# Optimization experiments

Hardware: AMD Instinct MI355X
Metric: run time of the kernel (lower is better)

Reference implementation:

```python
import jax, jax.numpy as jnp
import numpy as np

G, B, K, D = 16384, 4, 2, 64
NEG = -1e30


def _mlp3(x, w1, b1, w2, b2, w3, b3):
    # MLP: linear->relu x3 (BatchNorm defined but unused in original forward)
    h = jax.nn.relu(x @ w1 + b1)
    h = jax.nn.relu(h @ w2 + b2)
    return jax.nn.relu(h @ w3 + b3)


def setup_inputs() -> dict:
    key = jax.random.key(0)
    ks = jax.random.split(key, 32)

    def lin(k, fan_in, fan_out):
        k1, k2 = jax.random.split(k)
        s = 1.0 / np.sqrt(fan_in)
        w = jax.random.uniform(k1, (fan_in, fan_out), jnp.float32, -s, s)
        b = jax.random.uniform(k2, (fan_out,), jnp.float32, -s, s)
        return w, b

    inp = {}
    inp['ap_feat'] = jax.random.normal(ks[0], (G, B, 1), jnp.float32)
    inp['e_feat'] = jax.random.normal(ks[1], (G, B, K, 2), jnp.float32)
    inp['w_pre_ap'], inp['b_pre_ap'] = lin(ks[2], 1, D)
    inp['w_pre_edge'], inp['b_pre_edge'] = lin(ks[3], 2, D)
    # mlp_update_5 (AP-side neighbor messages), _6 (UE-side), _7 (edge update)
    inp['w5_1'], inp['b5_1'] = lin(ks[4], 2 * D, D)
    inp['w5_2'], inp['b5_2'] = lin(ks[5], D, D)
    inp['w5_3'], inp['b5_3'] = lin(ks[6], D, D)
    inp['w6_1'], inp['b6_1'] = lin(ks[7], 2 * D, D)
    inp['w6_2'], inp['b6_2'] = lin(ks[8], D, D)
    inp['w6_3'], inp['b6_3'] = lin(ks[9], D, D)
    inp['w7_1'], inp['b7_1'] = lin(ks[10], 2 * D, D)
    inp['w7_2'], inp['b7_2'] = lin(ks[11], D, D)
    inp['w7_3'], inp['b7_3'] = lin(ks[12], D, D)
    inp['w_post'], inp['b_post'] = lin(ks[13], D, 2)
    return inp


def _edge_conv(e, a, w5_1, b5_1, w5_2, b5_2, w5_3, b5_3,
               w6_1, b6_1, w6_2, b6_2, w6_3, b6_3,
               w7_1, b7_1, w7_2, b7_2, w7_3, b7_3):
    # e: [G,B,K,D] AP2UE edge hid; a: [G,B,D] AP hid.
    # M1[g,b,j] = mlp5(cat(a[g,b], e[g,b,j])) -- same-AP neighbor edges
    x1 = jnp.concatenate([jnp.broadcast_to(a[:, :, None, :], e.shape), e], axis=-1)  # [G,B,K,2D]
    M1 = _mlp3(x1, w5_1, b5_1, w5_2, b5_2, w5_3, b5_3)  # [G,B,K,D]
    # M2[g,b,bp,k] = mlp6(cat(a[g,b], e[g,bp,k])) -- same-UE neighbor edges
    # (original uses the SRC AP feature here too). Split first linear to
    # avoid materializing the [G,B,B,K,2D] concat.
    h = jax.nn.relu(
        (a @ w6_1[:D])[:, :, None, None, :]
        + (e @ w6_1[D:])[:, None, :, :, :]
        + b6_1)  # [G,B,B,K,D]
    h = jax.nn.relu(h @ w6_2 + b6_2)
    M2 = jax.nn.relu(h @ w6_3 + b6_3)  # [G,B,Bp,K,D]
    # masked max excluding the edge itself
    eyeK = jnp.eye(K, dtype=bool)  # [k, j]
    m1max = jnp.max(jnp.where(eyeK[None, None, :, :, None], NEG,
                              M1[:, :, None, :, :]), axis=3)  # [G,B,K,D]
    eyeB = jnp.eye(B, dtype=bool)  # [b, bp]
    m2max = jnp.max(jnp.where(eyeB[None, :, :, None, None], NEG, M2), axis=2)  # [G,B,K,D]
    agg = jnp.maximum(m1max, m2max)
    # new edge feature: mlp7(cat(agg, e_hid))
    return _mlp3(jnp.concatenate([agg, e], axis=-1),
                 w7_1, b7_1, w7_2, b7_2, w7_3, b7_3)


def reference(ap_feat, e_feat, w_pre_ap, b_pre_ap, w_pre_edge, b_pre_edge,
              w5_1, b5_1, w5_2, b5_2, w5_3, b5_3,
              w6_1, b6_1, w6_2, b6_2, w6_3, b6_3,
              w7_1, b7_1, w7_2, b7_2, w7_3, b7_3,
              w_post, b_post):
    # PreLayer (live branches only: AP nodes and AP2UE edges; APConv/UEConv
    # write node 'new' which is never read, so UE/UE2AP branches are dead).
    a = jax.nn.relu(ap_feat @ w_pre_ap + b_pre_ap)   # [G,B,D]
    e = jax.nn.relu(e_feat @ w_pre_edge + b_pre_edge)  # [G,B,K,D]
    # two UpdateLayers (shared weights: ModuleList([UpdateLayer()]*2) + global MLPs)
    for _ in range(2):
        e = _edge_conv(e, a, w5_1, b5_1, w5_2, b5_2, w5_3, b5_3,
                       w6_1, b6_1, w6_2, b6_2, w6_3, b6_3,
                       w7_1, b7_1, w7_2, b7_2, w7_3, b7_3)
    out = e @ w_post + b_post  # [G,B,K,2]
    r, im = out[..., 0], out[..., 1]
    # norm_func: per-graph [B,K] complex matrix, each row (over K) L2-normalized
    n = jnp.sqrt(jnp.sum(r * r + im * im, axis=-1, keepdims=True))
    return jnp.stack([r / n, im / n], axis=-1)  # [G,B,K,2]
```

## Files before the change

kernel.cpp:

```cpp
#include <hip/hip_runtime.h>


typedef unsigned short u16;
typedef unsigned int   u32;
typedef __attribute__((ext_vector_type(8))) short short8_t;
typedef __attribute__((ext_vector_type(2))) short short2v;
typedef __attribute__((ext_vector_type(4))) float floatx4;

#define OFF_W51 0
#define OFF_W61 8192
#define OFF_W71 16384
#define OFF_W52 24576
#define OFF_W53 28672
#define OFF_W62 32768
#define OFF_W63 36864
#define OFF_W72 40960
#define OFF_W73 45056
#define WS_U16  49152

#define CB51 0
#define CB52 64
#define CB53 128
#define CB61 192
#define CB62 256
#define CB63 320
#define CB71 384
#define CB72 448
#define CB73 512
#define CWPO 576
#define CBPO 704
#define CWPA 768
#define CBPA 832
#define CWPE 896
#define CBPE 1024
#define CSZ  1088

#define BUF_U16 1152
#define APB_U16 576
#define PW_U16  3456

struct Params {
  const float *ap, *ef;
  const float *wpa, *bpa, *wpe, *bpe;
  const float *w51, *b51, *w52, *b52, *w53, *b53;
  const float *w61, *b61, *w62, *b62, *w63, *b63;
  const float *w71, *b71, *w72, *b72, *w73, *b73;
  const float *wpost, *bpost;
  float *out;
  int gtot;
};

__device__ __forceinline__ u32 pk2(float a, float b) {
  const u32 ua = __float_as_uint(a) + 0x8000u;
  const u32 ub = __float_as_uint(b) + 0x8000u;
  return __builtin_amdgcn_perm(ub, ua, 0x07060302u);
}
__device__ __forceinline__ float blo(u32 v) { return __uint_as_float(v << 16); }
__device__ __forceinline__ float bhi(u32 v) { return __uint_as_float(v & 0xffff0000u); }
__device__ __forceinline__ u32 pkmax(u32 a, u32 b) {
  const short2v r = __builtin_elementwise_max(__builtin_bit_cast(short2v, a),
                                              __builtin_bit_cast(short2v, b));
  return __builtin_bit_cast(u32, r);
}
__device__ __forceinline__ u32 ror16(u32 x) { return (x >> 16) | (x << 16); }
__device__ __forceinline__ float sel4(int i, float x0, float x1, float x2, float x3) {
  const float lo = (i & 1) ? x1 : x0;
  const float hi = (i & 1) ? x3 : x2;
  return (i & 2) ? hi : lo;
}

__device__ __forceinline__ int skr(int row) { return row * 8 + (row >> 3) * 8; }

__device__ __forceinline__ floatx4 mfma16(short8_t a, short8_t b, floatx4 c) {
  return __builtin_amdgcn_mfma_f32_16x16x32_bf16(a, b, c, 0, 0, 0);
}
__device__ __forceinline__ short8_t ldAr(const u16* buf, int row) {
  return *(const short8_t*)(buf + skr(row));
}

template<int TSTRIDE>
__device__ __forceinline__ void layerK64R2(floatx4* aX, floatx4* aY,
                                           short8_t x0, short8_t x1,
                                           short8_t y0, short8_t y1,
                                           const u16* B, int l) {
#pragma unroll
  for (int t = 0; t < 4; ++t) {
    const short8_t b0 = *(const short8_t*)(B + (t * TSTRIDE + 0) * 512 + l * 8);
    const short8_t b1 = *(const short8_t*)(B + (t * TSTRIDE + 1) * 512 + l * 8);
    aX[t] = mfma16(x0, b0, aX[t]);
    aY[t] = mfma16(y0, b0, aY[t]);
    aX[t] = mfma16(x1, b1, aX[t]);
    aY[t] = mfma16(y1, b1, aY[t]);
  }
}

__device__ __forceinline__ void layerK128R2(floatx4* aX, floatx4* aY,
                                            const short8_t* fx, const short8_t* fy,
                                            const u16* B, int l) {
#pragma unroll
  for (int t = 0; t < 4; ++t)
#pragma unroll
    for (int h = 0; h < 4; ++h) {
      const short8_t b = *(const short8_t*)(B + (t * 4 + h) * 512 + l * 8);
      aX[t] = mfma16(fx[h], b, aX[t]);
      aY[t] = mfma16(fy[h], b, aY[t]);
    }
}

__device__ __forceinline__ void scatter_relu_bf16(u16* dst, const floatx4* acc, int q, int n) {
#pragma unroll
  for (int t = 0; t < 4; ++t) {
    const int kk = (t & 1) * 2 + (n >> 3);
    const int r0 = (t >> 1) * 64 + 4 * q + 16 * kk;
    u16* base = dst + (n & 7);
    const u32 v01 = pk2(fmaxf(acc[t][0], 0.f), fmaxf(acc[t][1], 0.f));
    const u32 v23 = pk2(fmaxf(acc[t][2], 0.f), fmaxf(acc[t][3], 0.f));
    base[skr(r0 + 0)] = (u16)v01;
    base[skr(r0 + 1)] = (u16)(v01 >> 16);
    base[skr(r0 + 2)] = (u16)v23;
    base[skr(r0 + 3)] = (u16)(v23 >> 16);
  }
}

__device__ __forceinline__ void scatter_bf16(u16* dst, const floatx4* acc, int q, int n) {
#pragma unroll
  for (int t = 0; t < 4; ++t) {
    const int kk = (t & 1) * 2 + (n >> 3);
    const int r0 = (t >> 1) * 64 + 4 * q + 16 * kk;
    u16* base = dst + (n & 7);
    const u32 v01 = pk2(acc[t][0], acc[t][1]);
    const u32 v23 = pk2(acc[t][2], acc[t][3]);
    base[skr(r0 + 0)] = (u16)v01;
    base[skr(r0 + 1)] = (u16)(v01 >> 16);
    base[skr(r0 + 2)] = (u16)v23;
    base[skr(r0 + 3)] = (u16)(v23 >> 16);
  }
}

__device__ __forceinline__ void scatter_pk(u16* dst, const u32* src, int q, int n) {
#pragma unroll
  for (int t = 0; t < 4; ++t) {
    const int kk = (t & 1) * 2 + (n >> 3);
    const int r0 = (t >> 1) * 64 + 4 * q + 16 * kk;
    u16* base = dst + (n & 7);
#pragma unroll
    for (int half = 0; half < 2; ++half) {
      const u32 v = src[2 * t + half];
      base[skr(r0 + 2 * half + 0)] = (u16)v;
      base[skr(r0 + 2 * half + 1)] = (u16)(v >> 16);
    }
  }
}

__device__ __forceinline__ void scatter_aP(u16* dst, const floatx4* acc, int q, int n,
                                           const float* cb61) {
#pragma unroll
  for (int t = 0; t < 4; ++t) {
    const int kk = (t & 1) * 2 + (n >> 3);
    const int r0 = (t >> 1) * 32 + 2 * q + 8 * kk;
    u16* base = dst + (n & 7);
    const float bv = cb61[16 * t + n];
    const u32 v = pk2(acc[t][0] + bv, acc[t][2] + bv);
    base[skr(r0 + 0)] = (u16)v;
    base[skr(r0 + 1)] = (u16)(v >> 16);
  }
}

__device__ __forceinline__ void init_accL(floatx4* acc, const float* cb, int n) {
#pragma unroll
  for (int t = 0; t < 4; ++t) {
    const float b = cb[16 * t + n];
    floatx4 v; v[0] = b; v[1] = b; v[2] = b; v[3] = b;
    acc[t] = v;
  }
}
__device__ __forceinline__ void init_acc0(floatx4* acc) {
#pragma unroll
  for (int t = 0; t < 4; ++t) { acc[t][0] = 0.f; acc[t][1] = 0.f; acc[t][2] = 0.f; acc[t][3] = 0.f; }
}

struct frag2 { short8_t f0, f1; };

__device__ __forceinline__ frag2 make_a(float apv, int q, const float* sc) {
  frag2 r;
#pragma unroll
  for (int h = 0; h < 2; ++h) {
    const int fb = 32 * h + 8 * q;
    const float4 wa0 = *(const float4*)(sc + CWPA + fb);
    const float4 wa1 = *(const float4*)(sc + CWPA + fb + 4);
    const float4 ba0 = *(const float4*)(sc + CBPA + fb);
    const float4 ba1 = *(const float4*)(sc + CBPA + fb + 4);
    uint4 pa;
    pa.x = pk2(fmaxf(fmaf(apv, wa0.x, ba0.x), 0.f), fmaxf(fmaf(apv, wa0.y, ba0.y), 0.f));
    pa.y = pk2(fmaxf(fmaf(apv, wa0.z, ba0.z), 0.f), fmaxf(fmaf(apv, wa0.w, ba0.w), 0.f));
    pa.z = pk2(fmaxf(fmaf(apv, wa1.x, ba1.x), 0.f), fmaxf(fmaf(apv, wa1.y, ba1.y), 0.f));
    pa.w = pk2(fmaxf(fmaf(apv, wa1.z, ba1.z), 0.f), fmaxf(fmaf(apv, wa1.w, ba1.w), 0.f));
    if (h == 0) r.f0 = __builtin_bit_cast(short8_t, pa);
    else        r.f1 = __builtin_bit_cast(short8_t, pa);
  }
  return r;
}

__device__ __forceinline__ void prelayer(frag2& A, short8_t& e0, short8_t& e1,
                                         const Params& p, const float* sc,
                                         int g0, int q, int n) {
  const float apv = p.ap[(g0 + (n >> 3)) * 4 + ((n >> 1) & 3)];
  A = make_a(apv, q, sc);
  const float f0 = p.ef[(g0 + (n >> 3)) * 16 + (n & 7) * 2];
  const float f1 = p.ef[(g0 + (n >> 3)) * 16 + (n & 7) * 2 + 1];
#pragma unroll
  for (int h = 0; h < 2; ++h) {
    const int fb = 32 * h + 8 * q;
    const float4 w00 = *(const float4*)(sc + CWPE + fb);
    const float4 w01 = *(const float4*)(sc + CWPE + fb + 4);
    const float4 w10 = *(const float4*)(sc + CWPE + 64 + fb);
    const float4 w11 = *(const float4*)(sc + CWPE + 64 + fb + 4);
    const float4 be0 = *(const float4*)(sc + CBPE + fb);
    const float4 be1 = *(const float4*)(sc + CBPE + fb + 4);
    uint4 pe;
    pe.x = pk2(fmaxf(fmaf(f0, w00.x, fmaf(f1, w10.x, be0.x)), 0.f),
               fmaxf(fmaf(f0, w00.y, fmaf(f1, w10.y, be0.y)), 0.f));
    pe.y = pk2(fmaxf(fmaf(f0, w00.z, fmaf(f1, w10.z, be0.z)), 0.f),
               fmaxf(fmaf(f0, w00.w, fmaf(f1, w10.w, be0.w)), 0.f));
    pe.z = pk2(fmaxf(fmaf(f0, w01.x, fmaf(f1, w11.x, be1.x)), 0.f),
               fmaxf(fmaf(f0, w01.y, fmaf(f1, w11.y, be1.y)), 0.f));
    pe.w = pk2(fmaxf(fmaf(f0, w01.z, fmaf(f1, w11.z, be1.z)), 0.f),
               fmaxf(fmaf(f0, w01.w, fmaf(f1, w11.w, be1.w)), 0.f));
    if (h == 0) e0 = __builtin_bit_cast(short8_t, pe);
    else        e1 = __builtin_bit_cast(short8_t, pe);
  }
}

__device__ __forceinline__ void build_h(short8_t* hf0, short8_t* hf1,
                                        const u16* aPb, const u16* BUF,
                                        int q, int n) {
  const int d = n >> 1;
  const int b_ln = d & 3;
  const uint4 av0 = *(const uint4*)(aPb + skr(0 * 32 + d + 8 * q));
  const uint4 av1 = *(const uint4*)(aPb + skr(1 * 32 + d + 8 * q));
#pragma unroll
  for (int j = 0; j < 3; ++j) {
    const int bp = j + (j >= b_ln);
    const int re = (n & 8) + bp * 2 + (n & 1);
#pragma unroll
    for (int h = 0; h < 2; ++h) {
      const uint4 av = h ? av1 : av0;
      const uint4 ev = *(const uint4*)(BUF + skr(h * 64 + re + 16 * q));
      uint4 ph;
      ph.x = pk2(fmaxf(blo(av.x) + blo(ev.x), 0.f),
                 fmaxf(bhi(av.x) + bhi(ev.x), 0.f));
      ph.y = pk2(fmaxf(blo(av.y) + blo(ev.y), 0.f),
                 fmaxf(bhi(av.y) + bhi(ev.y), 0.f));
      ph.z = pk2(fmaxf(blo(av.z) + blo(ev.z), 0.f),
                 fmaxf(bhi(av.z) + bhi(ev.z), 0.f));
      ph.w = pk2(fmaxf(blo(av.w) + blo(ev.w), 0.f),
                 fmaxf(bhi(av.w) + bhi(ev.w), 0.f));
      if (h == 0) hf0[j] = __builtin_bit_cast(short8_t, ph);
      else        hf1[j] = __builtin_bit_cast(short8_t, ph);
    }
  }
}

__device__ __forceinline__ void epilogue(const floatx4* acc3, const float* sc,
                                         float* out, int g0, int q, int n, bool ok) {
  float prr[4] = {0.f, 0.f, 0.f, 0.f}, pii[4] = {0.f, 0.f, 0.f, 0.f};
#pragma unroll
  for (int t = 0; t < 4; ++t) {
    const float wr = sc[CWPO + (16 * t + n) * 2];
    const float wi = sc[CWPO + (16 * t + n) * 2 + 1];
#pragma unroll
    for (int r = 0; r < 4; ++r) {
      const float e = fmaxf(acc3[t][r], 0.f);
      prr[r] = fmaf(e, wr, prr[r]);
      pii[r] = fmaf(e, wi, pii[r]);
    }
  }
  const float bpR = sc[CBPO], bpI = sc[CBPO + 1];
#pragma unroll
  for (int r = 0; r < 4; ++r) {
#pragma unroll
    for (int off = 1; off < 16; off <<= 1) {
      prr[r] += __shfl_xor(prr[r], off, 16);
      pii[r] += __shfl_xor(pii[r], off, 16);
    }
    prr[r] += bpR;
    pii[r] += bpI;
  }
  const int r = n >> 1, c = n & 1, rp = r ^ 1;
  const float pr_r  = sel4(r,  prr[0], prr[1], prr[2], prr[3]);
  const float pi_r  = sel4(r,  pii[0], pii[1], pii[2], pii[3]);
  const float pr_rp = sel4(rp, prr[0], prr[1], prr[2], prr[3]);
  const float pi_rp = sel4(rp, pii[0], pii[1], pii[2], pii[3]);
  const float num = c ? pi_r : pr_r;
  const float n2  = pr_r * pr_r + pi_r * pi_r + pr_rp * pr_rp + pi_rp * pi_rp;
  if (ok && n < 8) out[g0 * 16 + (4 * q + r) * 2 + c] = num / sqrtf(n2);
}

#define NBLK 256
#define NWAVE 8
#define PPW  2

__global__ __launch_bounds__(512, 2)
__attribute__((amdgpu_waves_per_eu(2, 2)))
void hetgnn_mfma(Params p) {
  __shared__ __align__(16) u16   sW[WS_U16];
  __shared__ __align__(16) u16   sAct[NWAVE * PW_U16];
  __shared__ __align__(16) float sConst[CSZ];

  const int tid  = threadIdx.x;
  const int wave = tid >> 6;
  const int l    = tid & 63;
  const int q    = l >> 4;
  const int n    = l & 15;

  {
    for (int fi = wave; fi < 96; fi += NWAVE) {
      int t, h, mi;
      if (fi < 48) { mi = fi >> 4; const int loc = fi & 15; t = loc >> 2; h = loc & 3; }
      else { const int j = fi - 48; mi = 3 + (j >> 3); const int loc = j & 7; t = loc >> 1; h = loc & 1; }
      const float* W =
          (mi == 0) ? p.w51 : (mi == 1) ? p.w61 : (mi == 2) ? p.w71 :
          (mi == 3) ? p.w52 : (mi == 4) ? p.w53 : (mi == 5) ? p.w62 :
          (mi == 6) ? p.w63 : (mi == 7) ? p.w72 : p.w73;
      const int nn = 16 * t + n;
      const int k0 = 32 * h + q * 8;
      float w[8];
#pragma unroll
      for (int j = 0; j < 8; ++j) w[j] = W[(k0 + j) * 64 + nn];
      uint4 o;
      o.x = pk2(w[0], w[1]); o.y = pk2(w[2], w[3]);
      o.z = pk2(w[4], w[5]); o.w = pk2(w[6], w[7]);
      *(uint4*)(sW + fi * 512 + l * 8) = o;
    }
  }
  if (tid < 64) {
    sConst[CB51 + tid] = p.b51[tid];
    sConst[CB52 + tid] = p.b52[tid];
    sConst[CB53 + tid] = p.b53[tid];
    sConst[CB61 + tid] = p.b61[tid];
    sConst[CB62 + tid] = p.b62[tid];
    sConst[CB63 + tid] = p.b63[tid];
    sConst[CB71 + tid] = p.b71[tid];
    sConst[CB72 + tid] = p.b72[tid];
    sConst[CB73 + tid] = p.b73[tid];
    sConst[CWPA + tid] = p.wpa[tid];
    sConst[CBPA + tid] = p.bpa[tid];
    sConst[CBPE + tid] = p.bpe[tid];
  }
  if (tid < 128) {
    sConst[CWPO + tid] = p.wpost[tid];
    sConst[CWPE + tid] = p.wpe[tid];
  }
  if (tid < 2) sConst[CBPO + tid] = p.bpost[tid];
  __syncthreads();

  u16* BUF0 = sAct + wave * PW_U16;
  u16* aPb0 = BUF0 + BUF_U16;
  u16* BUF1 = aPb0 + APB_U16;
  u16* aPb1 = BUF1 + BUF_U16;

  const int wslot = blockIdx.x * NWAVE + wave;

#pragma unroll 1
  for (int pi = 0; pi < PPW; ++pi) {
    const int g0X = (wslot * 4 + 2 * pi) * 2;
    const int g0Y = g0X + 2;
    if (g0X + 2 > p.gtot) break;
    const bool okY = (g0Y + 2 <= p.gtot);
    const int gY  = okY ? g0Y : g0X;

    frag2 AX, AY;
    short8_t ex0, ex1, ey0, ey1;
    prelayer(AX, ex0, ex1, p, sConst, g0X, q, n);
    prelayer(AY, ey0, ey1, p, sConst, gY,  q, n);

    {
      floatx4 aaX[4], aaY[4];
      init_acc0(aaX); init_acc0(aaY);
      layerK64R2<4>(aaX, aaY, AX.f0, AX.f1, AY.f0, AY.f1, sW + OFF_W61, l);
      scatter_aP(aPb0, aaX, q, n, sConst + CB61);
      scatter_aP(aPb1, aaY, q, n, sConst + CB61);
    }

#pragma unroll 1
    for (int it = 0; it < 2; ++it) {
      if (it == 1) {
        ex0 = ldAr(BUF0, l); ex1 = ldAr(BUF0, 64 + l);
        ey0 = ldAr(BUF1, l); ey1 = ldAr(BUF1, 64 + l);
      }

      u32 m1pX[8], m1pY[8];
      {
        floatx4 aX[4], aY[4];
        init_accL(aX, sConst + CB51, n); init_accL(aY, sConst + CB51, n);
        const short8_t fx[4] = {AX.f0, AX.f1, ex0, ex1};
        const short8_t fy[4] = {AY.f0, AY.f1, ey0, ey1};
        layerK128R2(aX, aY, fx, fy, sW + OFF_W51, l);
        scatter_relu_bf16(BUF0, aX, q, n);
        scatter_relu_bf16(BUF1, aY, q, n);
        floatx4 bX[4], bY[4];
        init_accL(bX, sConst + CB52, n); init_accL(bY, sConst + CB52, n);
        {
          const short8_t gx0 = ldAr(BUF0, l), gx1 = ldAr(BUF0, 64 + l);
          const short8_t gy0 = ldAr(BUF1, l), gy1 = ldAr(BUF1, 64 + l);
          layerK64R2<2>(bX, bY, gx0, gx1, gy0, gy1, sW + OFF_W52, l);
        }
        scatter_relu_bf16(BUF0, bX, q, n);
        scatter_relu_bf16(BUF1, bY, q, n);
        floatx4 cX[4], cY[4];
        init_accL(cX, sConst + CB53, n); init_accL(cY, sConst + CB53, n);
        {
          const short8_t gx0 = ldAr(BUF0, l), gx1 = ldAr(BUF0, 64 + l);
          const short8_t gy0 = ldAr(BUF1, l), gy1 = ldAr(BUF1, 64 + l);
          layerK64R2<2>(cX, cY, gx0, gx1, gy0, gy1, sW + OFF_W53, l);
        }
#pragma unroll
        for (int t = 0; t < 4; ++t) {
          m1pX[2 * t + 0] = pk2(cX[t][0], cX[t][1]);
          m1pX[2 * t + 1] = pk2(cX[t][2], cX[t][3]);
          m1pY[2 * t + 0] = pk2(cY[t][0], cY[t][1]);
          m1pY[2 * t + 1] = pk2(cY[t][2], cY[t][3]);
        }
      }

      u32 m2pX[8], m2pY[8];
      {
        floatx4 eX[4], eY[4];
        init_acc0(eX); init_acc0(eY);
        layerK64R2<4>(eX, eY, ex0, ex1, ey0, ey1, sW + OFF_W61 + 2 * 512, l);
        scatter_bf16(BUF0, eX, q, n);
        scatter_bf16(BUF1, eY, q, n);

        short8_t hfX0[3], hfX1[3], hfY0[3], hfY1[3];
        build_h(hfX0, hfX1, aPb0, BUF0, q, n);
        build_h(hfY0, hfY1, aPb1, BUF1, q, n);

#pragma unroll
        for (int j = 0; j < 3; ++j) {
          floatx4 uX[4], uY[4];
          init_accL(uX, sConst + CB62, n); init_accL(uY, sConst + CB62, n);
          layerK64R2<2>(uX, uY, hfX0[j], hfX1[j], hfY0[j], hfY1[j], sW + OFF_W62, l);
          scatter_relu_bf16(BUF0, uX, q, n);
          scatter_relu_bf16(BUF1, uY, q, n);
          floatx4 vX[4], vY[4];
          init_accL(vX, sConst + CB63, n); init_accL(vY, sConst + CB63, n);
          {
            const short8_t gx0 = ldAr(BUF0, l), gx1 = ldAr(BUF0, 64 + l);
            const short8_t gy0 = ldAr(BUF1, l), gy1 = ldAr(BUF1, 64 + l);
            layerK64R2<2>(vX, vY, gx0, gx1, gy0, gy1, sW + OFF_W63, l);
          }
#pragma unroll
          for (int t = 0; t < 4; ++t) {
#pragma unroll
            for (int h = 0; h < 2; ++h) {
              const u32 cX = pk2(vX[t][2 * h], vX[t][2 * h + 1]);
              const u32 cY = pk2(vY[t][2 * h], vY[t][2 * h + 1]);
              m2pX[2 * t + h] = (j == 0) ? cX : pkmax(m2pX[2 * t + h], cX);
              m2pY[2 * t + h] = (j == 0) ? cY : pkmax(m2pY[2 * t + h], cY);
            }
          }
        }
      }

      {
        u32 agX[8], agY[8];
#pragma unroll
        for (int i = 0; i < 8; ++i) {
          agX[i] = pkmax(pkmax(ror16(m1pX[i]), m2pX[i]), 0u);
          agY[i] = pkmax(pkmax(ror16(m1pY[i]), m2pY[i]), 0u);
        }
        scatter_pk(BUF0, agX, q, n);
        scatter_pk(BUF1, agY, q, n);
        floatx4 aX[4], aY[4];
        init_accL(aX, sConst + CB71, n); init_accL(aY, sConst + CB71, n);
        {
          const short8_t gx0 = ldAr(BUF0, l), gx1 = ldAr(BUF0, 64 + l);
          const short8_t gy0 = ldAr(BUF1, l), gy1 = ldAr(BUF1, 64 + l);
          const short8_t fx[4] = {gx0, gx1, ex0, ex1};
          const short8_t fy[4] = {gy0, gy1, ey0, ey1};
          layerK128R2(aX, aY, fx, fy, sW + OFF_W71, l);
        }
        scatter_relu_bf16(BUF0, aX, q, n);
        scatter_relu_bf16(BUF1, aY, q, n);
        floatx4 bX[4], bY[4];
        init_accL(bX, sConst + CB72, n); init_accL(bY, sConst + CB72, n);
        {
          const short8_t gx0 = ldAr(BUF0, l), gx1 = ldAr(BUF0, 64 + l);
          const short8_t gy0 = ldAr(BUF1, l), gy1 = ldAr(BUF1, 64 + l);
          layerK64R2<2>(bX, bY, gx0, gx1, gy0, gy1, sW + OFF_W72, l);
        }
        scatter_relu_bf16(BUF0, bX, q, n);
        scatter_relu_bf16(BUF1, bY, q, n);
        floatx4 cX[4], cY[4];
        init_accL(cX, sConst + CB73, n); init_accL(cY, sConst + CB73, n);
        {
          const short8_t gx0 = ldAr(BUF0, l), gx1 = ldAr(BUF0, 64 + l);
          const short8_t gy0 = ldAr(BUF1, l), gy1 = ldAr(BUF1, 64 + l);
          layerK64R2<2>(cX, cY, gx0, gx1, gy0, gy1, sW + OFF_W73, l);
        }

        if (it == 0) {
          scatter_relu_bf16(BUF0, cX, q, n);
          scatter_relu_bf16(BUF1, cY, q, n);
        } else {
          epilogue(cX, sConst, p.out, g0X, q, n, true);
          epilogue(cY, sConst, p.out, g0Y, q, n, okY);
        }
      }
    }
  }
}

extern "C" void kernel_launch(void* const* d_in, const int* in_sizes, int n_in,
                              void* d_out, int out_size, void* d_ws, size_t ws_size,
                              hipStream_t stream) {
  Params p;
  p.ap    = (const float*)d_in[0];
  p.ef    = (const float*)d_in[1];
  p.wpa   = (const float*)d_in[2];  p.bpa   = (const float*)d_in[3];
  p.wpe   = (const float*)d_in[4];  p.bpe   = (const float*)d_in[5];
  p.w51   = (const float*)d_in[6];  p.b51   = (const float*)d_in[7];
  p.w52   = (const float*)d_in[8];  p.b52   = (const float*)d_in[9];
  p.w53   = (const float*)d_in[10]; p.b53   = (const float*)d_in[11];
  p.w61   = (const float*)d_in[12]; p.b61   = (const float*)d_in[13];
  p.w62   = (const float*)d_in[14]; p.b62   = (const float*)d_in[15];
  p.w63   = (const float*)d_in[16]; p.b63   = (const float*)d_in[17];
  p.w71   = (const float*)d_in[18]; p.b71   = (const float*)d_in[19];
  p.w72   = (const float*)d_in[20]; p.b72   = (const float*)d_in[21];
  p.w73   = (const float*)d_in[22]; p.b73   = (const float*)d_in[23];
  p.wpost = (const float*)d_in[24]; p.bpost = (const float*)d_in[25];
  p.out   = (float*)d_out;
  p.gtot  = in_sizes[0] / 4;

  hipLaunchKernelGGL(hetgnn_mfma, dim3(NBLK), dim3(512), 0, stream, p);
}
```

Baseline: 166.9 us.

## Permute hidden-feature order so LDS activation scatters use packed 32-bit stores

Renumbers the K dimension of the first-layer, second and third MLP weights and the pre-layer constants so each lane's two MFMA output columns sit adjacent in LDS. Activation scatter and ReLU can then write one packed 32-bit word instead of two 16-bit stores, which halves LDS store instructions between layers. The LDS row padding changes as well, and compiler memory fences are added after the scatters. The risk is a mismatch in the permuted index mapping, which would silently corrupt results.

```diff
diff --git a/kernel.cpp b/kernel.cpp
--- a/kernel.cpp
+++ b/kernel.cpp
@@ -6,6 +6,8 @@
 typedef __attribute__((ext_vector_type(8))) short short8_t;
 typedef __attribute__((ext_vector_type(2))) short short2v;
 typedef __attribute__((ext_vector_type(4))) float floatx4;
+
+#define LDSFENCE() asm volatile("" ::: "memory")
 
 #define OFF_W51 0
 #define OFF_W61 8192
@@ -62,7 +64,6 @@
                                               __builtin_bit_cast(short2v, b));
   return __builtin_bit_cast(u32, r);
 }
-__device__ __forceinline__ u32 ror16(u32 x) { return (x >> 16) | (x << 16); }
 __device__ __forceinline__ float sel4(int i, float x0, float x1, float x2, float x3) {
   const float lo = (i & 1) ? x1 : x0;
   const float hi = (i & 1) ? x3 : x2;
@@ -74,8 +75,9 @@
 __device__ __forceinline__ floatx4 mfma16(short8_t a, short8_t b, floatx4 c) {
   return __builtin_amdgcn_mfma_f32_16x16x32_bf16(a, b, c, 0, 0, 0);
 }
-__device__ __forceinline__ short8_t ldAr(const u16* buf, int row) {
-  return *(const short8_t*)(buf + skr(row));
+__device__ __forceinline__ short8_t ldN(const u16* buf, int row) {
+  const uint4 v = *(const uint4*)(buf + row * 8 + (row >> 4) * 8);
+  return __builtin_bit_cast(short8_t, v);
 }
 
 template<int TSTRIDE>
@@ -107,19 +109,30 @@
     }
 }
 
-__device__ __forceinline__ void scatter_relu_bf16(u16* dst, const floatx4* acc, int q, int n) {
-#pragma unroll
-  for (int t = 0; t < 4; ++t) {
-    const int kk = (t & 1) * 2 + (n >> 3);
-    const int r0 = (t >> 1) * 64 + 4 * q + 16 * kk;
-    u16* base = dst + (n & 7);
-    const u32 v01 = pk2(fmaxf(acc[t][0], 0.f), fmaxf(acc[t][1], 0.f));
-    const u32 v23 = pk2(fmaxf(acc[t][2], 0.f), fmaxf(acc[t][3], 0.f));
-    base[skr(r0 + 0)] = (u16)v01;
-    base[skr(r0 + 1)] = (u16)(v01 >> 16);
-    base[skr(r0 + 2)] = (u16)v23;
-    base[skr(r0 + 3)] = (u16)(v23 >> 16);
-  }
+__device__ __forceinline__ void scatterN_relu(u16* dst, const floatx4* acc, int q, int n) {
+  u32* d32 = (u32*)dst;
+  const int g = n >> 2, d = n & 3;
+#pragma unroll
+  for (int tp = 0; tp < 2; ++tp)
+#pragma unroll
+    for (int r = 0; r < 4; ++r) {
+      const int row = tp * 64 + g * 16 + 4 * q + r;
+      d32[row * 4 + (row >> 4) * 4 + d] =
+          pkmax(pk2(acc[2 * tp + 0][r], acc[2 * tp + 1][r]), 0u);
+    }
+  LDSFENCE();
+}
+__device__ __forceinline__ void scatterN_u32(u16* dst, const u32* v, int q, int n) {
+  u32* d32 = (u32*)dst;
+  const int g = n >> 2, d = n & 3;
+#pragma unroll
+  for (int tp = 0; tp < 2; ++tp)
+#pragma unroll
+    for (int r = 0; r < 4; ++r) {
+      const int row = tp * 64 + g * 16 + 4 * q + r;
+      d32[row * 4 + (row >> 4) * 4 + d] = v[tp * 4 + r];
+    }
+  LDSFENCE();
 }
 
 __device__ __forceinline__ void scatter_bf16(u16* dst, const floatx4* acc, int q, int n) {
@@ -135,21 +148,7 @@
     base[skr(r0 + 2)] = (u16)v23;
     base[skr(r0 + 3)] = (u16)(v23 >> 16);
   }
-}
-
-__device__ __forceinline__ void scatter_pk(u16* dst, const u32* src, int q, int n) {
-#pragma unroll
-  for (int t = 0; t < 4; ++t) {
-    const int kk = (t & 1) * 2 + (n >> 3);
-    const int r0 = (t >> 1) * 64 + 4 * q + 16 * kk;
-    u16* base = dst + (n & 7);
-#pragma unroll
-    for (int half = 0; half < 2; ++half) {
-      const u32 v = src[2 * t + half];
-      base[skr(r0 + 2 * half + 0)] = (u16)v;
-      base[skr(r0 + 2 * half + 1)] = (u16)(v >> 16);
-    }
-  }
+  LDSFENCE();
 }
 
 __device__ __forceinline__ void scatter_aP(u16* dst, const floatx4* acc, int q, int n,
@@ -164,6 +163,7 @@
     base[skr(r0 + 0)] = (u16)v;
     base[skr(r0 + 1)] = (u16)(v >> 16);
   }
+  LDSFENCE();
 }
 
 __device__ __forceinline__ void init_accL(floatx4* acc, const float* cb, int n) {
@@ -323,10 +323,15 @@
           (mi == 3) ? p.w52 : (mi == 4) ? p.w53 : (mi == 5) ? p.w62 :
           (mi == 6) ? p.w63 : (mi == 7) ? p.w72 : p.w73;
       const int nn = 16 * t + n;
-      const int k0 = 32 * h + q * 8;
       float w[8];
 #pragma unroll
-      for (int j = 0; j < 8; ++j) w[j] = W[(k0 + j) * 64 + nn];
+      for (int jj = 0; jj < 8; ++jj) {
+        int kidx;
+        if (fi < 48)      kidx = 64 * (h >> 1) + 32 * (h & 1) + (jj & 1) * 16 + 4 * q + (jj >> 1);
+        else if (mi == 5) kidx = 32 * h + 8 * q + jj;
+        else              kidx = 32 * h + (jj & 1) * 16 + 4 * q + (jj >> 1);
+        w[jj] = W[kidx * 64 + nn];
+      }
       uint4 o;
       o.x = pk2(w[0], w[1]); o.y = pk2(w[2], w[3]);
       o.z = pk2(w[4], w[5]); o.w = pk2(w[6], w[7]);
@@ -343,13 +348,16 @@
     sConst[CB71 + tid] = p.b71[tid];
     sConst[CB72 + tid] = p.b72[tid];
     sConst[CB73 + tid] = p.b73[tid];
-    sConst[CWPA + tid] = p.wpa[tid];
-    sConst[CBPA + tid] = p.bpa[tid];
-    sConst[CBPE + tid] = p.bpe[tid];
+    const int feat = 32 * (tid >> 5) + (tid & 1) * 16 + 4 * ((tid >> 3) & 3) + ((tid >> 1) & 3);
+    sConst[CWPA + tid] = p.wpa[feat];
+    sConst[CBPA + tid] = p.bpa[feat];
+    sConst[CBPE + tid] = p.bpe[feat];
   }
   if (tid < 128) {
     sConst[CWPO + tid] = p.wpost[tid];
-    sConst[CWPE + tid] = p.wpe[tid];
+    const int s = tid & 63;
+    const int feat = 32 * (s >> 5) + (s & 1) * 16 + 4 * ((s >> 3) & 3) + ((s >> 1) & 3);
+    sConst[CWPE + tid] = p.wpe[(tid >> 6) * 64 + feat];
   }
   if (tid < 2) sConst[CBPO + tid] = p.bpost[tid];
   __syncthreads();
@@ -385,8 +393,8 @@
 #pragma unroll 1
     for (int it = 0; it < 2; ++it) {
       if (it == 1) {
-        ex0 = ldAr(BUF0, l); ex1 = ldAr(BUF0, 64 + l);
-        ey0 = ldAr(BUF1, l); ey1 = ldAr(BUF1, 64 + l);
+        ex0 = ldN(BUF0, l); ex1 = ldN(BUF0, 64 + l);
+        ey0 = ldN(BUF1, l); ey1 = ldN(BUF1, 64 + l);
       }
 
       u32 m1pX[8], m1pY[8];
@@ -396,31 +404,31 @@
         const short8_t fx[4] = {AX.f0, AX.f1, ex0, ex1};
         const short8_t fy[4] = {AY.f0, AY.f1, ey0, ey1};
         layerK128R2(aX, aY, fx, fy, sW + OFF_W51, l);
-        scatter_relu_bf16(BUF0, aX, q, n);
-        scatter_relu_bf16(BUF1, aY, q, n);
+        scatterN_relu(BUF0, aX, q, n);
+        scatterN_relu(BUF1, aY, q, n);
         floatx4 bX[4], bY[4];
         init_accL(bX, sConst + CB52, n); init_accL(bY, sConst + CB52, n);
         {
-          const short8_t gx0 = ldAr(BUF0, l), gx1 = ldAr(BUF0, 64 + l);
-          const short8_t gy0 = ldAr(BUF1, l), gy1 = ldAr(BUF1, 64 + l);
+          const short8_t gx0 = ldN(BUF0, l), gx1 = ldN(BUF0, 64 + l);
+          const short8_t gy0 = ldN(BUF1, l), gy1 = ldN(BUF1, 64 + l);
           layerK64R2<2>(bX, bY, gx0, gx1, gy0, gy1, sW + OFF_W52, l);
         }
-        scatter_relu_bf16(BUF0, bX, q, n);
-        scatter_relu_bf16(BUF1, bY, q, n);
+        scatterN_relu(BUF0, bX, q, n);
+        scatterN_relu(BUF1, bY, q, n);
         floatx4 cX[4], cY[4];
         init_accL(cX, sConst + CB53, n); init_accL(cY, sConst + CB53, n);
         {
-          const short8_t gx0 = ldAr(BUF0, l), gx1 = ldAr(BUF0, 64 + l);
-          const short8_t gy0 = ldAr(BUF1, l), gy1 = ldAr(BUF1, 64 + l);
+          const short8_t gx0 = ldN(BUF0, l), gx1 = ldN(BUF0, 64 + l);
+          const short8_t gy0 = ldN(BUF1, l), gy1 = ldN(BUF1, 64 + l);
           layerK64R2<2>(cX, cY, gx0, gx1, gy0, gy1, sW + OFF_W53, l);
         }
 #pragma unroll
-        for (int t = 0; t < 4; ++t) {
-          m1pX[2 * t + 0] = pk2(cX[t][0], cX[t][1]);
-          m1pX[2 * t + 1] = pk2(cX[t][2], cX[t][3]);
-          m1pY[2 * t + 0] = pk2(cY[t][0], cY[t][1]);
-          m1pY[2 * t + 1] = pk2(cY[t][2], cY[t][3]);
-        }
+        for (int tp = 0; tp < 2; ++tp)
+#pragma unroll
+          for (int r = 0; r < 4; ++r) {
+            m1pX[tp * 4 + r] = pk2(cX[2 * tp][r], cX[2 * tp + 1][r]);
+            m1pY[tp * 4 + r] = pk2(cY[2 * tp][r], cY[2 * tp + 1][r]);
+          }
       }
 
       u32 m2pX[8], m2pY[8];
@@ -440,68 +448,71 @@
           floatx4 uX[4], uY[4];
           init_accL(uX, sConst + CB62, n); init_accL(uY, sConst + CB62, n);
           layerK64R2<2>(uX, uY, hfX0[j], hfX1[j], hfY0[j], hfY1[j], sW + OFF_W62, l);
-          scatter_relu_bf16(BUF0, uX, q, n);
-          scatter_relu_bf16(BUF1, uY, q, n);
+          scatterN_relu(BUF0, uX, q, n);
+          scatterN_relu(BUF1, uY, q, n);
           floatx4 vX[4], vY[4];
           init_accL(vX, sConst + CB63, n); init_accL(vY, sConst + CB63, n);
           {
-            const short8_t gx0 = ldAr(BUF0, l), gx1 = ldAr(BUF0, 64 + l);
-            const short8_t gy0 = ldAr(BUF1, l), gy1 = ldAr(BUF1, 64 + l);
+            const short8_t gx0 = ldN(BUF0, l), gx1 = ldN(BUF0, 64 + l);
+            const short8_t gy0 = ldN(BUF1, l), gy1 = ldN(BUF1, 64 + l);
             layerK64R2<2>(vX, vY, gx0, gx1, gy0, gy1, sW + OFF_W63, l);
           }
 #pragma unroll
-          for (int t = 0; t < 4; ++t) {
-#pragma unroll
-            for (int h = 0; h < 2; ++h) {
-              const u32 cX = pk2(vX[t][2 * h], vX[t][2 * h + 1]);
-              const u32 cY = pk2(vY[t][2 * h], vY[t][2 * h + 1]);
-              m2pX[2 * t + h] = (j == 0) ? cX : pkmax(m2pX[2 * t + h], cX);
-              m2pY[2 * t + h] = (j == 0) ? cY : pkmax(m2pY[2 * t + h], cY);
+          for (int tp = 0; tp < 2; ++tp)
+#pragma unroll
+            for (int r = 0; r < 4; ++r) {
+              const u32 cXv = pk2(vX[2 * tp][r], vX[2 * tp + 1][r]);
+              const u32 cYv = pk2(vY[2 * tp][r], vY[2 * tp + 1][r]);
+              const int i = tp * 4 + r;
+              m2pX[i] = (j == 0) ? cXv : pkmax(m2pX[i], cXv);
+              m2pY[i] = (j == 0) ? cYv : pkmax(m2pY[i], cYv);
             }
-          }
         }
       }
 
       {
         u32 agX[8], agY[8];
 #pragma unroll
-        for (int i = 0; i < 8; ++i) {
-          agX[i] = pkmax(pkmax(ror16(m1pX[i]), m2pX[i]), 0u);
-          agY[i] = pkmax(pkmax(ror16(m1pY[i]), m2pY[i]), 0u);
-        }
-        scatter_pk(BUF0, agX, q, n);
-        scatter_pk(BUF1, agY, q, n);
+        for (int tp = 0; tp < 2; ++tp)
+#pragma unroll
+          for (int r = 0; r < 4; ++r) {
+            const int i = tp * 4 + r;
+            agX[i] = pkmax(pkmax(m1pX[tp * 4 + (r ^ 1)], m2pX[i]), 0u);
+            agY[i] = pkmax(pkmax(m1pY[tp * 4 + (r ^ 1)], m2pY[i]), 0u);
+          }
+        scatterN_u32(BUF0, agX, q, n);
+        scatterN_u32(BUF1, agY, q, n);
         floatx4 aX[4], aY[4];
         init_accL(aX, sConst + CB71, n); init_accL(aY, sConst + CB71, n);
         {
-          const short8_t gx0 = ldAr(BUF0, l), gx1 = ldAr(BUF0, 64 + l);
-          const short8_t gy0 = ldAr(BUF1, l), gy1 = ldAr(BUF1, 64 + l);
+          const short8_t gx0 = ldN(BUF0, l), gx1 = ldN(BUF0, 64 + l);
+          const short8_t gy0 = ldN(BUF1, l), gy1 = ldN(BUF1, 64 + l);
           const short8_t fx[4] = {gx0, gx1, ex0, ex1};
           const short8_t fy[4] = {gy0, gy1, ey0, ey1};
           layerK128R2(aX, aY, fx, fy, sW + OFF_W71, l);
         }
-        scatter_relu_bf16(BUF0, aX, q, n);
-        scatter_relu_bf16(BUF1, aY, q, n);
+        scatterN_relu(BUF0, aX, q, n);
+        scatterN_relu(BUF1, aY, q, n);
         floatx4 bX[4], bY[4];
         init_accL(bX, sConst + CB72, n); init_accL(bY, sConst + CB72, n);
         {
-          const short8_t gx0 = ldAr(BUF0, l), gx1 = ldAr(BUF0, 64 + l);
-          const short8_t gy0 = ldAr(BUF1, l), gy1 = ldAr(BUF1, 64 + l);
+          const short8_t gx0 = ldN(BUF0, l), gx1 = ldN(BUF0, 64 + l);
+          const short8_t gy0 = ldN(BUF1, l), gy1 = ldN(BUF1, 64 + l);
           layerK64R2<2>(bX, bY, gx0, gx1, gy0, gy1, sW + OFF_W72, l);
         }
-        scatter_relu_bf16(BUF0, bX, q, n);
-        scatter_relu_bf16(BUF1, bY, q, n);
+        scatterN_relu(BUF0, bX, q, n);
+        scatterN_relu(BUF1, bY, q, n);
         floatx4 cX[4], cY[4];
         init_accL(cX, sConst + CB73, n); init_accL(cY, sConst + CB73, n);
         {
-          const short8_t gx0 = ldAr(BUF0, l), gx1 = ldAr(BUF0, 64 + l);
-          const short8_t gy0 = ldAr(BUF1, l), gy1 = ldAr(BUF1, 64 + l);
+          const short8_t gx0 = ldN(BUF0, l), gx1 = ldN(BUF0, 64 + l);
+          const short8_t gy0 = ldN(BUF1, l), gy1 = ldN(BUF1, 64 + l);
           layerK64R2<2>(cX, cY, gx0, gx1, gy0, gy1, sW + OFF_W73, l);
         }
 
         if (it == 0) {
-          scatter_relu_bf16(BUF0, cX, q, n);
-          scatter_relu_bf16(BUF1, cY, q, n);
+          scatterN_relu(BUF0, cX, q, n);
+          scatterN_relu(BUF1, cY, q, n);
         } else {
           epilogue(cX, sConst, p.out, g0X, q, n, true);
           epilogue(cY, sConst, p.out, g0Y, q, n, okY);
```

After: 157.2 us. 1.06x faster.
